# Performance work log

Hardware: AMD Instinct MI355X
Metric: run time of the kernel (lower is better)

The kernel has to match this reference:

```python
import jax, jax.numpy as jnp
import numpy as np

NUM_DEPTH_BINS = 64
EPS_PROJ = 1e-8   # added to z before perspective divide (Project3D)
EPS_DIV = 1e-4    # view-count normalizer eps in cost volume reduction


def _bilinear_zeros(feat_flat, x, y, H, W):
    """grid_sample(mode=bilinear, padding=zeros, align_corners=False).
    feat_flat: (Bv, C, H*W); x, y: (Bv, M) continuous pixel coords (already shifted by -0.5)."""
    Bv, C, _ = feat_flat.shape
    M = x.shape[1]
    x0 = jnp.floor(x)
    y0 = jnp.floor(y)

    def g(xi, yi):
        valid = (xi >= 0) & (xi <= W - 1) & (yi >= 0) & (yi <= H - 1)
        xi_c = jnp.clip(xi, 0, W - 1).astype(jnp.int32)
        yi_c = jnp.clip(yi, 0, H - 1).astype(jnp.int32)
        idx = (yi_c * W + xi_c)[:, None, :]  # (Bv,1,M)
        vals = jnp.take_along_axis(feat_flat, jnp.broadcast_to(idx, (Bv, C, M)), axis=2)
        return vals * valid[:, None, :].astype(feat_flat.dtype)

    wx1 = (x - x0)[:, None, :]
    wy1 = (y - y0)[:, None, :]
    wx0 = 1.0 - wx1
    wy0 = 1.0 - wy1
    return (g(x0, y0) * wx0 * wy0 + g(x0 + 1.0, y0) * wx1 * wy0
            + g(x0, y0 + 1.0) * wx0 * wy1 + g(x0 + 1.0, y0 + 1.0) * wx1 * wy1)


def setup_inputs() -> dict:
    B, S, C, H, W = 1, 7, 16, 64, 96
    key = jax.random.key(0)
    k1, k2 = jax.random.split(key)
    cur_feats = jax.random.normal(k1, (B, C, H, W), jnp.float32)
    src_feats = jax.random.normal(k2, (B, S, C, H, W), jnp.float32)

    fx = fy = 1.2 * W
    cx, cy = W / 2.0, H / 2.0
    K = np.array([[fx, 0, cx, 0], [0, fy, cy, 0], [0, 0, 1, 0], [0, 0, 0, 1]], np.float32)

    rng = np.random.RandomState(0)
    ext = np.zeros((B, S, 4, 4), np.float32)
    for b in range(B):
        for s in range(S):
            axis = rng.normal(size=3)
            axis /= np.linalg.norm(axis)
            ang = rng.uniform(-0.05, 0.05)
            Kx = np.array([[0, -axis[2], axis[1]], [axis[2], 0, -axis[0]], [-axis[1], axis[0], 0]])
            R = np.eye(3) + np.sin(ang) * Kx + (1 - np.cos(ang)) * (Kx @ Kx)
            T = np.eye(4, dtype=np.float32)
            T[:3, :3] = R
            T[:3, 3] = rng.uniform(-0.08, 0.08, 3)
            ext[b, s] = T

    return {
        'cur_feats': cur_feats,
        'src_feats': src_feats,
        'src_extrinsics': jnp.asarray(ext),
        'src_poses': jnp.asarray(np.linalg.inv(ext).astype(np.float32)),
        'src_Ks': jnp.broadcast_to(jnp.asarray(K), (B, S, 4, 4)),
        'cur_invK': jnp.broadcast_to(jnp.asarray(np.linalg.inv(K).astype(np.float32)), (B, 4, 4)),
        'min_depth': jnp.full((B, 1, 1, 1), 0.25, jnp.float32),
        'max_depth': jnp.full((B, 1, 1, 1), 5.0, jnp.float32),
    }


def reference(cur_feats, src_feats, src_extrinsics, src_poses, src_Ks, cur_invK, min_depth, max_depth):
    del src_poses  # unused by the plain dot-product cost volume (as in torch code)
    B, S, C, H, W = src_feats.shape
    D = NUM_DEPTH_BINS
    dt = src_feats.dtype
    N = H * W

    # log-spaced depth planes, identical at every pixel: (B, D)
    ramp = jnp.linspace(0.0, 1.0, D, dtype=dt).reshape(1, D, 1, 1)
    depth_planes_bd = jnp.exp(jnp.log(min_depth) + jnp.log(max_depth / min_depth) * ramp)[:, :, 0, 0]

    # backproject: half-pixel-centered homogeneous grid -> camera rays
    yy, xx = jnp.meshgrid(jnp.arange(H, dtype=dt), jnp.arange(W, dtype=dt), indexing='ij')
    pix = jnp.stack([xx.ravel() + 0.5, yy.ravel() + 0.5, jnp.ones(N, dt)], axis=0)  # (3,N)
    rays = jnp.einsum('bij,jn->bin', cur_invK[:, :3, :3], pix)                      # (B,3,N)
    world = rays[:, None, :, :] * depth_planes_bd[:, :, None, None]                 # (B,D,3,N)
    world_h = jnp.concatenate([world, jnp.ones((B, D, 1, N), dt)], axis=2)          # (B,D,4,N)

    # project into every source view: P = K @ cam_T_world
    P = jnp.einsum('bsij,bsjk->bsik', src_Ks, src_extrinsics)[:, :, :3, :]          # (B,S,3,4)
    cam = jnp.einsum('bsij,bdjn->bsdin', P, world_h)                                # (B,S,D,3,N)
    z = cam[:, :, :, 2, :]
    px = cam[:, :, :, 0, :] / (z + EPS_PROJ)
    py = cam[:, :, :, 1, :] / (z + EPS_PROJ)

    # uv = 2*pix/size - 1 with align_corners=False  ==>  sample location = pix - 0.5
    x = (px - 0.5).reshape(B * S, D * N)
    y = (py - 0.5).reshape(B * S, D * N)
    feat_flat = src_feats.reshape(B * S, C, N)
    warped = _bilinear_zeros(feat_flat, x, y, H, W).reshape(B, S, C, D, H, W)

    mask = (z > 0).astype(dt).reshape(B, S, D, H, W)  # point in front of source cam
    dot = jnp.einsum('bscdhw,bchw->bsdhw', warped, cur_feats) * mask
    cost_volume = dot.sum(axis=1) / (mask.sum(axis=1) + EPS_DIV)  # (B,D,H,W)
    return cost_volume
```

## Files before the change

### kernel.cpp

```cpp
#include <hip/hip_runtime.h>

#define S_ 7
#define C_ 16
#define H_ 64
#define W_ 96
#define N_ (H_*W_)
#define D_ 64
#define EPS_PROJ 1e-8f
#define EPS_DIV  1e-4f

__global__ __launch_bounds__(256) void transpose_all(const float* __restrict__ src,
                                                     const float* __restrict__ cur,
                                                     float* __restrict__ src_t,
                                                     float* __restrict__ cur_t) {
    int tid = blockIdx.x * 256 + threadIdx.x;
    const int nsrc = S_ * C_ * N_;
    if (tid < nsrc) {
        int c = tid & (C_ - 1);
        int t = tid >> 4;
        int n = t % N_;
        int s = t / N_;
        src_t[tid] = src[(s * C_ + c) * N_ + n];
    } else {
        int u = tid - nsrc;
        if (u < C_ * N_) {
            int c = u & (C_ - 1);
            int n = u >> 4;
            cur_t[u] = cur[c * N_ + n];
        }
    }
}

__global__ __launch_bounds__(256, 3) void cost_volume_quad_d(
    const float* __restrict__ src_t,
    const float* __restrict__ cur_t,
    const float* __restrict__ Ks,
    const float* __restrict__ ext,
    const float* __restrict__ invK,
    const float* __restrict__ mind_p,
    const float* __restrict__ maxd_p,
    float* __restrict__ out)
{
    __shared__ float sP[S_][12];

    int t = threadIdx.x;
    if (t < S_ * 12) {
        int s = t / 12, e = t % 12, r = e >> 2, c = e & 3;
        float acc = 0.f;
#pragma unroll
        for (int j = 0; j < 4; ++j)
            acc += Ks[s * 16 + r * 4 + j] * ext[s * 16 + j * 4 + c];
        sP[s][e] = acc;
    }
    __syncthreads();

    int l4 = t & 3;
    int d  = t >> 2;
    int n0 = blockIdx.x * 4;
    int n  = n0 + l4;
    int w = n % W_, h = n / W_;

    float mind = mind_p[0], maxd = maxd_p[0];
    float depth = expf(logf(mind) + logf(maxd / mind) * ((float)d / (float)(D_ - 1)));

    float pxc = w + 0.5f, pyc = h + 0.5f;
    float rx = invK[0] * pxc + invK[1] * pyc + invK[2];
    float ry = invK[4] * pxc + invK[5] * pyc + invK[6];
    float rz = invK[8] * pxc + invK[9] * pyc + invK[10];

    float wx = rx * depth, wy = ry * depth, wz = rz * depth;

    float4 cfq[4];
#pragma unroll
    for (int j = 0; j < 4; ++j)
        cfq[j] = *(const float4*)(cur_t + (n0 + j) * C_ + l4 * 4);

    float pc[4] = {0.f, 0.f, 0.f, 0.f};
    float mcnt = 0.f;

#pragma unroll
    for (int s = 0; s < S_; ++s) {
        const float* p = sP[s];
        float cx = p[0] * wx + p[1] * wy + p[2]  * wz + p[3];
        float cy = p[4] * wx + p[5] * wy + p[6]  * wz + p[7];
        float cz = p[8] * wx + p[9] * wy + p[10] * wz + p[11];

        float iz = 1.f / (cz + EPS_PROJ);
        float x = cx * iz - 0.5f;
        float y = cy * iz - 0.5f;

        mcnt += (cz > 0.f) ? 1.f : 0.f;
        if (cz <= 0.f) { x = -1e8f; y = -1e8f; }

        const float* sf = src_t + s * (C_ * N_) + l4 * 4;

        float xj[4], yj[4];
#pragma unroll
        for (int j = 0; j < 4; ++j) {
            xj[j] = __shfl(x, j, 4);
            yj[j] = __shfl(y, j, 4);
        }

        int   off[16];
        float wgt[16];
#pragma unroll
        for (int j = 0; j < 4; ++j) {
            float x0f = floorf(xj[j]), y0f = floorf(yj[j]);
            float fx1 = xj[j] - x0f,  fy1 = yj[j] - y0f;
            float fx0 = 1.f - fx1, fy0 = 1.f - fy1;
            float x1f = x0f + 1.f, y1f = y0f + 1.f;

            float vx0 = (x0f >= 0.f && x0f <= (float)(W_ - 1)) ? fx0 : 0.f;
            float vx1 = (x1f >= 0.f && x1f <= (float)(W_ - 1)) ? fx1 : 0.f;
            float vy0 = (y0f >= 0.f && y0f <= (float)(H_ - 1)) ? fy0 : 0.f;
            float vy1 = (y1f >= 0.f && y1f <= (float)(H_ - 1)) ? fy1 : 0.f;

            int ix0 = (int)fminf(fmaxf(x0f, 0.f), (float)(W_ - 1));
            int ix1 = (int)fminf(fmaxf(x1f, 0.f), (float)(W_ - 1));
            int iy0 = (int)fminf(fmaxf(y0f, 0.f), (float)(H_ - 1));
            int iy1 = (int)fminf(fmaxf(y1f, 0.f), (float)(H_ - 1));

            int r0 = iy0 * W_, r1 = iy1 * W_;
            off[j * 4 + 0] = (r0 + ix0) * C_;
            off[j * 4 + 1] = (r0 + ix1) * C_;
            off[j * 4 + 2] = (r1 + ix0) * C_;
            off[j * 4 + 3] = (r1 + ix1) * C_;
            wgt[j * 4 + 0] = vx0 * vy0;
            wgt[j * 4 + 1] = vx1 * vy0;
            wgt[j * 4 + 2] = vx0 * vy1;
            wgt[j * 4 + 3] = vx1 * vy1;
        }

        float4 g[16];
#pragma unroll
        for (int k = 0; k < 16; ++k)
            g[k] = *(const float4*)(sf + off[k]);

#pragma unroll
        for (int j = 0; j < 4; ++j) {
            float4 cq = cfq[j];
#pragma unroll
            for (int c = 0; c < 4; ++c) {
                float4 gv = g[j * 4 + c];
                float dt = gv.x * cq.x + gv.y * cq.y + gv.z * cq.z + gv.w * cq.w;
                pc[j] += wgt[j * 4 + c] * dt;
            }
        }
    }

#pragma unroll
    for (int j = 0; j < 4; ++j) {
        pc[j] += __shfl_xor(pc[j], 1, 4);
        pc[j] += __shfl_xor(pc[j], 2, 4);
    }
    float total = (l4 == 0) ? pc[0] : (l4 == 1) ? pc[1] : (l4 == 2) ? pc[2] : pc[3];
    out[d * N_ + n0 + l4] = total / (mcnt + EPS_DIV);
}

__global__ __launch_bounds__(256) void cost_volume_scalar(
    const float* __restrict__ src, const float* __restrict__ cur,
    const float* __restrict__ Ks, const float* __restrict__ ext,
    const float* __restrict__ invK,
    const float* __restrict__ mind_p, const float* __restrict__ maxd_p,
    float* __restrict__ out)
{
    __shared__ float sP[S_][12];
    __shared__ float sdepth;
    int t = threadIdx.x;
    if (t < S_ * 12) {
        int s = t / 12, e = t % 12, r = e >> 2, c = e & 3;
        float acc = 0.f;
#pragma unroll
        for (int j = 0; j < 4; ++j)
            acc += Ks[s * 16 + r * 4 + j] * ext[s * 16 + j * 4 + c];
        sP[s][e] = acc;
    }
    if (t == 0) {
        int d = (blockIdx.x * 256) / N_;
        float mind = mind_p[0], maxd = maxd_p[0];
        sdepth = expf(logf(mind) + logf(maxd / mind) * ((float)d / (float)(D_ - 1)));
    }
    __syncthreads();

    int tid = blockIdx.x * 256 + t;
    int n = tid % N_;
    int w = n % W_, h = n / W_;
    float pxc = w + 0.5f, pyc = h + 0.5f;
    float rx = invK[0] * pxc + invK[1] * pyc + invK[2];
    float ry = invK[4] * pxc + invK[5] * pyc + invK[6];
    float rz = invK[8] * pxc + invK[9] * pyc + invK[10];
    float depth = sdepth;
    float wx = rx * depth, wy = ry * depth, wz = rz * depth;

    float cf[16];
#pragma unroll
    for (int c = 0; c < 16; ++c) cf[c] = cur[c * N_ + n];

    float cost = 0.f, mcnt = 0.f;
#pragma unroll
    for (int s = 0; s < S_; ++s) {
        const float* p = sP[s];
        float cx = p[0] * wx + p[1] * wy + p[2]  * wz + p[3];
        float cy = p[4] * wx + p[5] * wy + p[6]  * wz + p[7];
        float cz = p[8] * wx + p[9] * wy + p[10] * wz + p[11];
        float iz = 1.f / (cz + EPS_PROJ);
        float x = cx * iz - 0.5f;
        float y = cy * iz - 0.5f;
        float x0f = floorf(x), y0f = floorf(y);
        float fx1 = x - x0f, fy1 = y - y0f;
        float fx0 = 1.f - fx1, fy0 = 1.f - fy1;
        const float* sf = src + (size_t)s * (C_ * N_);
        float dsum = 0.f;
        float ys[2] = {y0f, y0f + 1.f}, wys[2] = {fy0, fy1};
        float xs[2] = {x0f, x0f + 1.f}, wxs[2] = {fx0, fx1};
#pragma unroll
        for (int ci = 0; ci < 2; ++ci) {
            float yf = ys[ci];
            if (!(yf >= 0.f && yf <= (float)(H_ - 1))) continue;
            int rowbase = (int)yf * W_;
#pragma unroll
            for (int cj = 0; cj < 2; ++cj) {
                float xf = xs[cj];
                if (xf >= 0.f && xf <= (float)(W_ - 1)) {
                    int idx = rowbase + (int)xf;
                    float dotp = 0.f;
#pragma unroll
                    for (int c = 0; c < 16; ++c) dotp += sf[c * N_ + idx] * cf[c];
                    dsum += wxs[cj] * wys[ci] * dotp;
                }
            }
        }
        float m = (cz > 0.f) ? 1.f : 0.f;
        cost += m * dsum;
        mcnt += m;
    }
    out[tid] = cost / (mcnt + EPS_DIV);
}

extern "C" void kernel_launch(void* const* d_in, const int* in_sizes, int n_in,
                              void* d_out, int out_size, void* d_ws, size_t ws_size,
                              hipStream_t stream) {
    const float* cur  = (const float*)d_in[0];
    const float* src  = (const float*)d_in[1];
    const float* ext  = (const float*)d_in[2];
    const float* Ks   = (const float*)d_in[4];
    const float* invK = (const float*)d_in[5];
    const float* mind = (const float*)d_in[6];
    const float* maxd = (const float*)d_in[7];
    float* out = (float*)d_out;

    const size_t need = (size_t)(S_ * N_ * C_ + N_ * C_) * sizeof(float);
    if (ws_size >= need) {
        float* src_t = (float*)d_ws;
        float* cur_t = src_t + (size_t)S_ * N_ * C_;
        const int tot = (S_ + 1) * C_ * N_;
        transpose_all<<<(tot + 255) / 256, 256, 0, stream>>>(src, cur, src_t, cur_t);
        cost_volume_quad_d<<<N_ / 4, 256, 0, stream>>>(
            src_t, cur_t, Ks, ext, invK, mind, maxd, out);
    } else {
        cost_volume_scalar<<<D_ * N_ / 256, 256, 0, stream>>>(
            src, cur, Ks, ext, invK, mind, maxd, out);
    }
}
```

Baseline: 98.83 us.

## Compute per-pixel projections redundantly, split gathers in halves, raise occupancy

Each lane now computes the projected coordinates for all four pixels of its quad itself, using a per-view per-unit-x delta vector stored in shared memory, instead of exchanging them with shuffles. The 16 gathered float4 loads per view are split into two batches of 8 to cut register pressure, and the launch bound asks for 4 blocks per CU instead of 3. The aim is higher occupancy to hide gather latency, at the cost of redundant projection arithmetic and fewer loads in flight per wave. Computing the coordinates incrementally can also change floating-point rounding slightly.

```diff
diff --git a/kernel.cpp b/kernel.cpp
--- a/kernel.cpp
+++ b/kernel.cpp
@@ -31,7 +31,7 @@
     }
 }
 
-__global__ __launch_bounds__(256, 3) void cost_volume_quad_d(
+__global__ __launch_bounds__(256, 4) void cost_volume_quad_d(
     const float* __restrict__ src_t,
     const float* __restrict__ cur_t,
     const float* __restrict__ Ks,
@@ -42,6 +42,7 @@
     float* __restrict__ out)
 {
     __shared__ float sP[S_][12];
+    __shared__ float sE[S_][3];
 
     int t = threadIdx.x;
     if (t < S_ * 12) {
@@ -53,21 +54,25 @@
         sP[s][e] = acc;
     }
     __syncthreads();
+    if (t < S_ * 3) {
+        int s = t / 3, k = t % 3;
+        const float* p = sP[s] + k * 4;
+        sE[s][k] = p[0] * invK[0] + p[1] * invK[4] + p[2] * invK[8];
+    }
+    __syncthreads();
 
     int l4 = t & 3;
     int d  = t >> 2;
     int n0 = blockIdx.x * 4;
-    int n  = n0 + l4;
-    int w = n % W_, h = n / W_;
+    int w0 = n0 % W_, h = n0 / W_;
 
     float mind = mind_p[0], maxd = maxd_p[0];
     float depth = expf(logf(mind) + logf(maxd / mind) * ((float)d / (float)(D_ - 1)));
 
-    float pxc = w + 0.5f, pyc = h + 0.5f;
+    float pxc = w0 + 0.5f, pyc = h + 0.5f;
     float rx = invK[0] * pxc + invK[1] * pyc + invK[2];
     float ry = invK[4] * pxc + invK[5] * pyc + invK[6];
     float rz = invK[8] * pxc + invK[9] * pyc + invK[10];
-
     float wx = rx * depth, wy = ry * depth, wz = rz * depth;
 
     float4 cfq[4];
@@ -81,69 +86,79 @@
 #pragma unroll
     for (int s = 0; s < S_; ++s) {
         const float* p = sP[s];
-        float cx = p[0] * wx + p[1] * wy + p[2]  * wz + p[3];
-        float cy = p[4] * wx + p[5] * wy + p[6]  * wz + p[7];
-        float cz = p[8] * wx + p[9] * wy + p[10] * wz + p[11];
-
-        float iz = 1.f / (cz + EPS_PROJ);
-        float x = cx * iz - 0.5f;
-        float y = cy * iz - 0.5f;
-
-        mcnt += (cz > 0.f) ? 1.f : 0.f;
-        if (cz <= 0.f) { x = -1e8f; y = -1e8f; }
+        float cx0 = p[0] * wx + p[1] * wy + p[2]  * wz + p[3];
+        float cy0 = p[4] * wx + p[5] * wy + p[6]  * wz + p[7];
+        float cz0 = p[8] * wx + p[9] * wy + p[10] * wz + p[11];
+        float dx = sE[s][0] * depth;
+        float dy = sE[s][1] * depth;
+        float dz = sE[s][2] * depth;
+
+        float czl = cz0 + (float)l4 * dz;
+        mcnt += (czl > 0.f) ? 1.f : 0.f;
+
+        float xj[4], yj[4];
+#pragma unroll
+        for (int j = 0; j < 4; ++j) {
+            float cxj = cx0 + (float)j * dx;
+            float cyj = cy0 + (float)j * dy;
+            float czj = cz0 + (float)j * dz;
+            float iz = 1.f / (czj + EPS_PROJ);
+            float xx = cxj * iz - 0.5f;
+            float yy = cyj * iz - 0.5f;
+            if (czj <= 0.f) { xx = -1e8f; yy = -1e8f; }
+            xj[j] = xx; yj[j] = yy;
+        }
 
         const float* sf = src_t + s * (C_ * N_) + l4 * 4;
 
-        float xj[4], yj[4];
-#pragma unroll
-        for (int j = 0; j < 4; ++j) {
-            xj[j] = __shfl(x, j, 4);
-            yj[j] = __shfl(y, j, 4);
-        }
-
-        int   off[16];
-        float wgt[16];
-#pragma unroll
-        for (int j = 0; j < 4; ++j) {
-            float x0f = floorf(xj[j]), y0f = floorf(yj[j]);
-            float fx1 = xj[j] - x0f,  fy1 = yj[j] - y0f;
-            float fx0 = 1.f - fx1, fy0 = 1.f - fy1;
-            float x1f = x0f + 1.f, y1f = y0f + 1.f;
-
-            float vx0 = (x0f >= 0.f && x0f <= (float)(W_ - 1)) ? fx0 : 0.f;
-            float vx1 = (x1f >= 0.f && x1f <= (float)(W_ - 1)) ? fx1 : 0.f;
-            float vy0 = (y0f >= 0.f && y0f <= (float)(H_ - 1)) ? fy0 : 0.f;
-            float vy1 = (y1f >= 0.f && y1f <= (float)(H_ - 1)) ? fy1 : 0.f;
-
-            int ix0 = (int)fminf(fmaxf(x0f, 0.f), (float)(W_ - 1));
-            int ix1 = (int)fminf(fmaxf(x1f, 0.f), (float)(W_ - 1));
-            int iy0 = (int)fminf(fmaxf(y0f, 0.f), (float)(H_ - 1));
-            int iy1 = (int)fminf(fmaxf(y1f, 0.f), (float)(H_ - 1));
-
-            int r0 = iy0 * W_, r1 = iy1 * W_;
-            off[j * 4 + 0] = (r0 + ix0) * C_;
-            off[j * 4 + 1] = (r0 + ix1) * C_;
-            off[j * 4 + 2] = (r1 + ix0) * C_;
-            off[j * 4 + 3] = (r1 + ix1) * C_;
-            wgt[j * 4 + 0] = vx0 * vy0;
-            wgt[j * 4 + 1] = vx1 * vy0;
-            wgt[j * 4 + 2] = vx0 * vy1;
-            wgt[j * 4 + 3] = vx1 * vy1;
-        }
-
-        float4 g[16];
-#pragma unroll
-        for (int k = 0; k < 16; ++k)
-            g[k] = *(const float4*)(sf + off[k]);
-
-#pragma unroll
-        for (int j = 0; j < 4; ++j) {
-            float4 cq = cfq[j];
-#pragma unroll
-            for (int c = 0; c < 4; ++c) {
-                float4 gv = g[j * 4 + c];
-                float dt = gv.x * cq.x + gv.y * cq.y + gv.z * cq.z + gv.w * cq.w;
-                pc[j] += wgt[j * 4 + c] * dt;
+#pragma unroll
+        for (int half = 0; half < 2; ++half) {
+            int   off[8];
+            float wgt[8];
+#pragma unroll
+            for (int jj = 0; jj < 2; ++jj) {
+                int j = half * 2 + jj;
+                float x0f = floorf(xj[j]), y0f = floorf(yj[j]);
+                float fx1 = xj[j] - x0f,  fy1 = yj[j] - y0f;
+                float fx0 = 1.f - fx1, fy0 = 1.f - fy1;
+                float x1f = x0f + 1.f, y1f = y0f + 1.f;
+
+                float vx0 = (x0f >= 0.f && x0f <= (float)(W_ - 1)) ? fx0 : 0.f;
+                float vx1 = (x1f >= 0.f && x1f <= (float)(W_ - 1)) ? fx1 : 0.f;
+                float vy0 = (y0f >= 0.f && y0f <= (float)(H_ - 1)) ? fy0 : 0.f;
+                float vy1 = (y1f >= 0.f && y1f <= (float)(H_ - 1)) ? fy1 : 0.f;
+
+                int ix0 = (int)fminf(fmaxf(x0f, 0.f), (float)(W_ - 1));
+                int ix1 = (int)fminf(fmaxf(x1f, 0.f), (float)(W_ - 1));
+                int iy0 = (int)fminf(fmaxf(y0f, 0.f), (float)(H_ - 1));
+                int iy1 = (int)fminf(fmaxf(y1f, 0.f), (float)(H_ - 1));
+
+                int r0 = iy0 * W_, r1 = iy1 * W_;
+                off[jj * 4 + 0] = (r0 + ix0) * C_;
+                off[jj * 4 + 1] = (r0 + ix1) * C_;
+                off[jj * 4 + 2] = (r1 + ix0) * C_;
+                off[jj * 4 + 3] = (r1 + ix1) * C_;
+                wgt[jj * 4 + 0] = vx0 * vy0;
+                wgt[jj * 4 + 1] = vx1 * vy0;
+                wgt[jj * 4 + 2] = vx0 * vy1;
+                wgt[jj * 4 + 3] = vx1 * vy1;
+            }
+
+            float4 g[8];
+#pragma unroll
+            for (int k = 0; k < 8; ++k)
+                g[k] = *(const float4*)(sf + off[k]);
+
+#pragma unroll
+            for (int jj = 0; jj < 2; ++jj) {
+                int j = half * 2 + jj;
+                float4 cq = cfq[j];
+#pragma unroll
+                for (int c = 0; c < 4; ++c) {
+                    float4 gv = g[jj * 4 + c];
+                    float dt = gv.x * cq.x + gv.y * cq.y + gv.z * cq.z + gv.w * cq.w;
+                    pc[j] += wgt[jj * 4 + c] * dt;
+                }
             }
         }
     }
```

Result: no change. 100.7 us (+1.9%).

## Store transposed source features in fp16 and split bilinear taps across lanes

Applied to the files above, without the earlier changes.

The transpose kernel now writes the source features as half precision, which halves the bytes of the gathered feature table. In the cost-volume kernel, each lane of a 4-lane group now handles one x-corner and one 8-channel half of the taps. That cuts per-lane gathers from 16 float4 loads to 8 float4 loads of packed halves. The occupancy hint is raised from 3 to 4 blocks per CU. The trade-off is fp16 rounding of the source features, which could affect tolerance, plus extra conversion instructions.

```diff
diff --git a/kernel.cpp b/kernel.cpp
--- a/kernel.cpp
+++ b/kernel.cpp
@@ -1,4 +1,5 @@
 #include <hip/hip_runtime.h>
+#include <hip/hip_fp16.h>
 
 #define S_ 7
 #define C_ 16
@@ -9,10 +10,10 @@
 #define EPS_PROJ 1e-8f
 #define EPS_DIV  1e-4f
 
-__global__ __launch_bounds__(256) void transpose_all(const float* __restrict__ src,
-                                                     const float* __restrict__ cur,
-                                                     float* __restrict__ src_t,
-                                                     float* __restrict__ cur_t) {
+__global__ __launch_bounds__(256) void transpose_all_h(const float* __restrict__ src,
+                                                       const float* __restrict__ cur,
+                                                       __half* __restrict__ src_h,
+                                                       float* __restrict__ cur_t) {
     int tid = blockIdx.x * 256 + threadIdx.x;
     const int nsrc = S_ * C_ * N_;
     if (tid < nsrc) {
@@ -20,7 +21,7 @@
         int t = tid >> 4;
         int n = t % N_;
         int s = t / N_;
-        src_t[tid] = src[(s * C_ + c) * N_ + n];
+        src_h[tid] = __float2half(src[(s * C_ + c) * N_ + n]);
     } else {
         int u = tid - nsrc;
         if (u < C_ * N_) {
@@ -31,8 +32,8 @@
     }
 }
 
-__global__ __launch_bounds__(256, 3) void cost_volume_quad_d(
-    const float* __restrict__ src_t,
+__global__ __launch_bounds__(256, 4) void cost_volume_h(
+    const __half* __restrict__ src_h,
     const float* __restrict__ cur_t,
     const float* __restrict__ Ks,
     const float* __restrict__ ext,
@@ -55,6 +56,8 @@
     __syncthreads();
 
     int l4 = t & 3;
+    int q  = l4 & 1;
+    int cs = (l4 >> 1) & 1;
     int d  = t >> 2;
     int n0 = blockIdx.x * 4;
     int n  = n0 + l4;
@@ -67,15 +70,17 @@
     float rx = invK[0] * pxc + invK[1] * pyc + invK[2];
     float ry = invK[4] * pxc + invK[5] * pyc + invK[6];
     float rz = invK[8] * pxc + invK[9] * pyc + invK[10];
-
     float wx = rx * depth, wy = ry * depth, wz = rz * depth;
 
-    float4 cfq[4];
-#pragma unroll
-    for (int j = 0; j < 4; ++j)
-        cfq[j] = *(const float4*)(cur_t + (n0 + j) * C_ + l4 * 4);
-
-    float pc[4] = {0.f, 0.f, 0.f, 0.f};
+    float4 cfA[4], cfB[4];
+#pragma unroll
+    for (int j = 0; j < 4; ++j) {
+        const float* cp = cur_t + (n0 + j) * C_ + q * 8;
+        cfA[j] = *(const float4*)(cp);
+        cfB[j] = *(const float4*)(cp + 4);
+    }
+
+    float acc[4] = {0.f, 0.f, 0.f, 0.f};
     float mcnt = 0.f;
 
 #pragma unroll
@@ -92,8 +97,6 @@
         mcnt += (cz > 0.f) ? 1.f : 0.f;
         if (cz <= 0.f) { x = -1e8f; y = -1e8f; }
 
-        const float* sf = src_t + s * (C_ * N_) + l4 * 4;
-
         float xj[4], yj[4];
 #pragma unroll
         for (int j = 0; j < 4; ++j) {
@@ -101,60 +104,62 @@
             yj[j] = __shfl(y, j, 4);
         }
 
-        int   off[16];
-        float wgt[16];
+        const __half* sfh = src_h + (size_t)s * (N_ * C_);
+
+        int   off[8];
+        float wgt[8];
 #pragma unroll
         for (int j = 0; j < 4; ++j) {
             float x0f = floorf(xj[j]), y0f = floorf(yj[j]);
             float fx1 = xj[j] - x0f,  fy1 = yj[j] - y0f;
-            float fx0 = 1.f - fx1, fy0 = 1.f - fy1;
-            float x1f = x0f + 1.f, y1f = y0f + 1.f;
-
-            float vx0 = (x0f >= 0.f && x0f <= (float)(W_ - 1)) ? fx0 : 0.f;
-            float vx1 = (x1f >= 0.f && x1f <= (float)(W_ - 1)) ? fx1 : 0.f;
+            float fy0 = 1.f - fy1;
+            float y1f = y0f + 1.f;
+            float xsf = cs ? (x0f + 1.f) : x0f;
+            float fxs = cs ? fx1 : (1.f - fx1);
+            float vxs = (xsf >= 0.f && xsf <= (float)(W_ - 1)) ? fxs : 0.f;
             float vy0 = (y0f >= 0.f && y0f <= (float)(H_ - 1)) ? fy0 : 0.f;
             float vy1 = (y1f >= 0.f && y1f <= (float)(H_ - 1)) ? fy1 : 0.f;
 
-            int ix0 = (int)fminf(fmaxf(x0f, 0.f), (float)(W_ - 1));
-            int ix1 = (int)fminf(fmaxf(x1f, 0.f), (float)(W_ - 1));
+            int ixs = (int)fminf(fmaxf(xsf, 0.f), (float)(W_ - 1));
             int iy0 = (int)fminf(fmaxf(y0f, 0.f), (float)(H_ - 1));
             int iy1 = (int)fminf(fmaxf(y1f, 0.f), (float)(H_ - 1));
 
-            int r0 = iy0 * W_, r1 = iy1 * W_;
-            off[j * 4 + 0] = (r0 + ix0) * C_;
-            off[j * 4 + 1] = (r0 + ix1) * C_;
-            off[j * 4 + 2] = (r1 + ix0) * C_;
-            off[j * 4 + 3] = (r1 + ix1) * C_;
-            wgt[j * 4 + 0] = vx0 * vy0;
-            wgt[j * 4 + 1] = vx1 * vy0;
-            wgt[j * 4 + 2] = vx0 * vy1;
-            wgt[j * 4 + 3] = vx1 * vy1;
-        }
-
-        float4 g[16];
-#pragma unroll
-        for (int k = 0; k < 16; ++k)
-            g[k] = *(const float4*)(sf + off[k]);
+            off[j * 2 + 0] = (iy0 * W_ + ixs) * C_ + q * 8;
+            off[j * 2 + 1] = (iy1 * W_ + ixs) * C_ + q * 8;
+            wgt[j * 2 + 0] = vxs * vy0;
+            wgt[j * 2 + 1] = vxs * vy1;
+        }
+
+        float4 g[8];
+#pragma unroll
+        for (int k = 0; k < 8; ++k)
+            g[k] = *(const float4*)(sfh + off[k]);
 
 #pragma unroll
         for (int j = 0; j < 4; ++j) {
-            float4 cq = cfq[j];
-#pragma unroll
-            for (int c = 0; c < 4; ++c) {
-                float4 gv = g[j * 4 + c];
-                float dt = gv.x * cq.x + gv.y * cq.y + gv.z * cq.z + gv.w * cq.w;
-                pc[j] += wgt[j * 4 + c] * dt;
+            float4 a = cfA[j], b = cfB[j];
+#pragma unroll
+            for (int k2 = 0; k2 < 2; ++k2) {
+                float4 gv = g[j * 2 + k2];
+                const __half2* hp = (const __half2*)&gv;
+                float2 f0 = __half22float2(hp[0]);
+                float2 f1 = __half22float2(hp[1]);
+                float2 f2 = __half22float2(hp[2]);
+                float2 f3 = __half22float2(hp[3]);
+                float dt = f0.x * a.x + f0.y * a.y + f1.x * a.z + f1.y * a.w
+                         + f2.x * b.x + f2.y * b.y + f3.x * b.z + f3.y * b.w;
+                acc[j] += wgt[j * 2 + k2] * dt;
             }
         }
     }
 
 #pragma unroll
     for (int j = 0; j < 4; ++j) {
-        pc[j] += __shfl_xor(pc[j], 1, 4);
-        pc[j] += __shfl_xor(pc[j], 2, 4);
-    }
-    float total = (l4 == 0) ? pc[0] : (l4 == 1) ? pc[1] : (l4 == 2) ? pc[2] : pc[3];
-    out[d * N_ + n0 + l4] = total / (mcnt + EPS_DIV);
+        acc[j] += __shfl_xor(acc[j], 1, 4);
+        acc[j] += __shfl_xor(acc[j], 2, 4);
+    }
+    float total = (l4 == 0) ? acc[0] : (l4 == 1) ? acc[1] : (l4 == 2) ? acc[2] : acc[3];
+    out[d * N_ + n] = total / (mcnt + EPS_DIV);
 }
 
 __global__ __launch_bounds__(256) void cost_volume_scalar(
@@ -249,14 +254,15 @@
     const float* maxd = (const float*)d_in[7];
     float* out = (float*)d_out;
 
-    const size_t need = (size_t)(S_ * N_ * C_ + N_ * C_) * sizeof(float);
+    const size_t need = (size_t)S_ * N_ * C_ * sizeof(__half)
+                      + (size_t)N_ * C_ * sizeof(float);
     if (ws_size >= need) {
-        float* src_t = (float*)d_ws;
-        float* cur_t = src_t + (size_t)S_ * N_ * C_;
+        __half* src_h = (__half*)d_ws;
+        float*  cur_t = (float*)(src_h + (size_t)S_ * N_ * C_);
         const int tot = (S_ + 1) * C_ * N_;
-        transpose_all<<<(tot + 255) / 256, 256, 0, stream>>>(src, cur, src_t, cur_t);
-        cost_volume_quad_d<<<N_ / 4, 256, 0, stream>>>(
-            src_t, cur_t, Ks, ext, invK, mind, maxd, out);
+        transpose_all_h<<<(tot + 255) / 256, 256, 0, stream>>>(src, cur, src_h, cur_t);
+        cost_volume_h<<<N_ / 4, 256, 0, stream>>>(
+            src_h, cur_t, Ks, ext, invK, mind, maxd, out);
     } else {
         cost_volume_scalar<<<D_ * N_ / 256, 256, 0, stream>>>(
             src, cur, Ks, ext, invK, mind, maxd, out);
```

Measured after the change: 92.91 us. 1.06x faster.
